# Performance work log

Hardware: AMD Instinct MI355X
Metric: run time of the kernel (lower is better)

Reference implementation:

```python
import jax, jax.numpy as jnp
import numpy as np

T, B, IN_DIM = 512, 256, 256
H1, H = 512, 256          # fc hidden, GRU hidden
OUT_DIM = 18


def setup_inputs() -> dict:
    key = jax.random.key(0)
    ks = jax.random.split(key, 14)
    s = 0.05
    return {
        "x":      jax.random.normal(ks[0], (T, B, IN_DIM), dtype=jnp.float32),
        # fc1: Linear(IN_DIM,H1)+ReLU, Linear(H1,H)+ReLU
        "W_fc1a": jax.random.normal(ks[1], (H1, IN_DIM), dtype=jnp.float32) * s,
        "b_fc1a": jax.random.normal(ks[2], (H1,), dtype=jnp.float32) * s,
        "W_fc1b": jax.random.normal(ks[3], (H, H1), dtype=jnp.float32) * s,
        "b_fc1b": jax.random.normal(ks[4], (H,), dtype=jnp.float32) * s,
        # GRUCell(H, H): weights ordered [r, z, n] like torch
        "W_ih":   jax.random.normal(ks[5], (3 * H, H), dtype=jnp.float32) * s,
        "b_ih":   jax.random.normal(ks[6], (3 * H,), dtype=jnp.float32) * s,
        "W_hh":   jax.random.normal(ks[7], (3 * H, H), dtype=jnp.float32) * s,
        "b_hh":   jax.random.normal(ks[8], (3 * H,), dtype=jnp.float32) * s,
        # fc2: Linear(H,H1)+ReLU, Linear(H1,OUT_DIM)
        "W_fc2a": jax.random.normal(ks[9], (H1, H), dtype=jnp.float32) * s,
        "b_fc2a": jax.random.normal(ks[10], (H1,), dtype=jnp.float32) * s,
        "W_fc2b": jax.random.normal(ks[11], (OUT_DIM, H1), dtype=jnp.float32) * s,
        "b_fc2b": jax.random.normal(ks[12], (OUT_DIM,), dtype=jnp.float32) * s,
    }


def reference(x, W_fc1a, b_fc1a, W_fc1b, b_fc1b,
              W_ih, b_ih, W_hh, b_hh,
              W_fc2a, b_fc2a, W_fc2b, b_fc2b):
    batch = x.shape[1]
    h0 = jnp.zeros((batch, W_hh.shape[1]), dtype=x.dtype)

    def step(h, xt):
        # fc1 MLP
        a = jax.nn.relu(xt @ W_fc1a.T + b_fc1a)
        a = jax.nn.relu(a @ W_fc1b.T + b_fc1b)
        # GRUCell (torch gate order r, z, n)
        gi = a @ W_ih.T + b_ih            # [B, 3H]
        gh = h @ W_hh.T + b_hh            # [B, 3H]
        i_r, i_z, i_n = jnp.split(gi, 3, axis=-1)
        h_r, h_z, h_n = jnp.split(gh, 3, axis=-1)
        r = jax.nn.sigmoid(i_r + h_r)
        z = jax.nn.sigmoid(i_z + h_z)
        n = jnp.tanh(i_n + r * h_n)
        h_new = (1.0 - z) * n + z * h
        # fc2 head
        q = jax.nn.relu(h_new @ W_fc2a.T + b_fc2a) @ W_fc2b.T + b_fc2b
        return h_new, q

    _, qs = jax.lax.scan(step, h0, x)     # qs: [T, B, OUT_DIM]
    return qs
```

## Files before the change

kernel.cpp:

```cpp
#include <hip/hip_runtime.h>
#include <hip/hip_fp16.h>
#include <cstdio>

typedef unsigned short u16;
typedef __attribute__((ext_vector_type(8))) _Float16 f16x8;
typedef __attribute__((ext_vector_type(4))) float fv4;

#define TT 512
#define BB 256

__device__ __forceinline__ float us2f(u16 u) {
    union { u16 u; _Float16 h; } c; c.u = u; return (float)c.h;
}
__device__ __forceinline__ u16 f2us(float f) {
    union { u16 u; _Float16 h; } c; c.h = (_Float16)f; return c.u;
}

__device__ __forceinline__ void gl_lds16(const u16* g, u16* l) {
    __builtin_amdgcn_global_load_lds(
        (const __attribute__((address_space(1))) void*)g,
        (__attribute__((address_space(3))) void*)l, 16, 0, 0);
}

__global__ void cvt_f32_f16(const float* __restrict__ s, u16* __restrict__ d, int n) {
    long stride = (long)gridDim.x * blockDim.x * 8;
    for (long i = ((long)blockIdx.x * blockDim.x + threadIdx.x) * 8; i < n; i += stride) {
        f16x8 o;
#pragma unroll
        for (int j = 0; j < 8; ++j) o[j] = (_Float16)s[i + j];
        *(f16x8*)(d + i) = o;
    }
}

__global__ void bias_fold(const float* __restrict__ bih, const float* __restrict__ bhh,
                          float* __restrict__ bsum) {
    int i = blockIdx.x * blockDim.x + threadIdx.x;
    if (i < 768) bsum[i] = bih[i] + (i < 512 ? bhh[i] : 0.f);
}

__global__ void pack_whh(const float* __restrict__ W, u16* __restrict__ Wp) {
    int t = blockIdx.x * blockDim.x + threadIdx.x;
    int l = t & 63;
    int kt = (t >> 6) & 7;
    int jt = t >> 9;
    int j = jt * 16 + (l & 15);
    int k = kt * 32 + (l >> 4) * 8;
    f16x8 o;
#pragma unroll
    for (int i = 0; i < 8; ++i) o[i] = (_Float16)W[j * 256 + k + i];
    *(f16x8*)(Wp + (size_t)t * 8) = o;
}

__global__ void pack_w2b(const float* __restrict__ W, u16* __restrict__ Wp) {
    int t = blockIdx.x * blockDim.x + threadIdx.x;
    int l = t & 63;
    int kt = (t >> 6) & 15;
    int nt = t >> 10;
    int n = nt * 16 + (l & 15);
    int k = kt * 32 + (l >> 4) * 8;
    f16x8 o;
#pragma unroll
    for (int i = 0; i < 8; ++i)
        o[i] = (n < 18) ? (_Float16)W[n * 512 + k + i] : (_Float16)0.f;
    *(f16x8*)(Wp + (size_t)t * 8) = o;
}

__global__ __launch_bounds__(256) void gemm_bt(
    const u16* __restrict__ A, const u16* __restrict__ B,
    const float* __restrict__ bias, u16* __restrict__ C,
    int N, int K, int act)
{
    __shared__ u16 Ash[4096] __attribute__((aligned(16)));
    __shared__ u16 Bsh[4096] __attribute__((aligned(16)));
    const int tid = threadIdx.x;
    const int l = tid & 63, w = tid >> 6;
    const long m0 = (long)blockIdx.y * 128;
    const int n0 = blockIdx.x * 128;
    const int r = tid >> 2, c8 = (tid & 3) * 8;
    const u16* gA0 = A + (m0 + r) * K + c8;
    const u16* gA1 = A + (m0 + 64 + r) * K + c8;
    const u16* gB0 = B + (long)(n0 + r) * K + c8;
    const u16* gB1 = B + (long)(n0 + 64 + r) * K + c8;
    const int mb = (w >> 1) * 64, nb = (w & 1) * 64;
    const int mrow = l & 15, colq = (l >> 4) * 8;
    fv4 acc[4][4] = {};
    for (int k0 = 0; k0 < K; k0 += 32) {
        gl_lds16(gA0 + k0, &Ash[tid * 8]);
        gl_lds16(gA1 + k0, &Ash[2048 + tid * 8]);
        gl_lds16(gB0 + k0, &Bsh[tid * 8]);
        gl_lds16(gB1 + k0, &Bsh[2048 + tid * 8]);
        __syncthreads();
        f16x8 af[4], bf[4];
#pragma unroll
        for (int i = 0; i < 4; ++i)
            af[i] = *(const f16x8*)&Ash[(mb + i * 16 + mrow) * 32 + colq];
#pragma unroll
        for (int i = 0; i < 4; ++i)
            bf[i] = *(const f16x8*)&Bsh[(nb + i * 16 + mrow) * 32 + colq];
#pragma unroll
        for (int mt = 0; mt < 4; ++mt)
#pragma unroll
            for (int nt = 0; nt < 4; ++nt)
                acc[mt][nt] = __builtin_amdgcn_mfma_f32_16x16x32_f16(
                    af[mt], bf[nt], acc[mt][nt], 0, 0, 0);
        __syncthreads();
    }
    float bv[4];
#pragma unroll
    for (int nt = 0; nt < 4; ++nt) bv[nt] = bias[n0 + nb + nt * 16 + mrow];
    const int rq = (l >> 4) * 4;
#pragma unroll
    for (int mt = 0; mt < 4; ++mt)
#pragma unroll
        for (int nt = 0; nt < 4; ++nt)
#pragma unroll
            for (int i = 0; i < 4; ++i) {
                float v = acc[mt][nt][i] + bv[nt];
                if (act) v = fmaxf(v, 0.f);
                C[(m0 + mb + mt * 16 + rq + i) * (long)N + (n0 + nb + nt * 16 + mrow)] = f2us(v);
            }
}

__global__ __launch_bounds__(256) void gemm_gi(
    const u16* __restrict__ A, const u16* __restrict__ B,
    const float* __restrict__ bias, u16* __restrict__ GIp)
{
    __shared__ u16 Ash[4096] __attribute__((aligned(16)));
    __shared__ u16 Bsh[4096] __attribute__((aligned(16)));
    const int tid = threadIdx.x;
    const int l = tid & 63, w = tid >> 6;
    const long m0 = (long)blockIdx.y * 128;
    const int n0 = blockIdx.x * 128;
    const int r = tid >> 2, c8 = (tid & 3) * 8;
    const u16* gA0 = A + (m0 + r) * 256 + c8;
    const u16* gA1 = A + (m0 + 64 + r) * 256 + c8;
    const u16* gB0 = B + (long)(n0 + r) * 256 + c8;
    const u16* gB1 = B + (long)(n0 + 64 + r) * 256 + c8;
    const int mb = (w >> 1) * 64, nb = (w & 1) * 64;
    const int mrow = l & 15, colq = (l >> 4) * 8;
    fv4 acc[4][4] = {};
    for (int k0 = 0; k0 < 256; k0 += 32) {
        gl_lds16(gA0 + k0, &Ash[tid * 8]);
        gl_lds16(gA1 + k0, &Ash[2048 + tid * 8]);
        gl_lds16(gB0 + k0, &Bsh[tid * 8]);
        gl_lds16(gB1 + k0, &Bsh[2048 + tid * 8]);
        __syncthreads();
        f16x8 af[4], bf[4];
#pragma unroll
        for (int i = 0; i < 4; ++i)
            af[i] = *(const f16x8*)&Ash[(mb + i * 16 + mrow) * 32 + colq];
#pragma unroll
        for (int i = 0; i < 4; ++i)
            bf[i] = *(const f16x8*)&Bsh[(nb + i * 16 + mrow) * 32 + colq];
#pragma unroll
        for (int mt = 0; mt < 4; ++mt)
#pragma unroll
            for (int nt = 0; nt < 4; ++nt)
                acc[mt][nt] = __builtin_amdgcn_mfma_f32_16x16x32_f16(
                    af[mt], bf[nt], acc[mt][nt], 0, 0, 0);
        __syncthreads();
    }
    float bv[4];
#pragma unroll
    for (int nt = 0; nt < 4; ++nt) bv[nt] = bias[n0 + nb + nt * 16 + mrow];
    const int rq = (l >> 4) * 4;
#pragma unroll
    for (int mt = 0; mt < 4; ++mt)
#pragma unroll
        for (int nt = 0; nt < 4; ++nt)
#pragma unroll
            for (int i = 0; i < 4; ++i) {
                float v = acc[mt][nt][i] + bv[nt];
                int m = (int)(m0 + mb + mt * 16 + rq + i);
                int n = n0 + nb + nt * 16 + mrow;
                int t  = m >> 8, b = m & 255;
                int blk = b >> 4, rb = b & 15, q = rb >> 2, i2 = rb & 3;
                int g = n >> 8, c = n & 255, w2 = c >> 5, s = (c >> 4) & 1, cl = c & 15;
                size_t idx = ((((size_t)t * 16 + blk) * 8 + w2) * 64 + (q * 16 + cl)) * 24
                             + (g * 2 + s) * 4 + i2;
                GIp[idx] = f2us(v);
            }
}

__global__ __launch_bounds__(512, 2) void gru_seq4(
    const u16* __restrict__ Wp, const u16* __restrict__ GIp,
    const float* __restrict__ bhh, u16* __restrict__ Hout)
{
    __shared__ u16 h_sh[2][4096] __attribute__((aligned(16)));
    __shared__ u16 Wl[24576] __attribute__((aligned(16)));
    const int tid = threadIdx.x;
    const int l = tid & 63, w = tid >> 6;
    const int blk = blockIdx.x;
    const int bg = blk * 16;
    const int col = l & 15, quad = l >> 4;

    for (int i = tid; i < 4096; i += 512) h_sh[0][i] = 0;
    for (int idx = tid; idx < 3072; idx += 512)
        *(f16x8*)&Wl[(size_t)idx * 8] =
            *(const f16x8*)&Wp[(((size_t)(idx >> 6) * 8 + 7) * 64 + (idx & 63)) * 8];

    int jts[6];
#pragma unroll
    for (int g = 0; g < 3; ++g)
#pragma unroll
        for (int s = 0; s < 2; ++s) jts[g * 2 + s] = g * 16 + 2 * w + s;

    f16x8 wf[6][7];
#pragma unroll
    for (int u = 0; u < 6; ++u)
#pragma unroll
        for (int kt = 0; kt < 7; ++kt)
            wf[u][kt] = *(const f16x8*)&Wp[(((size_t)jts[u] * 8 + kt) * 64 + l) * 8];

    float hbn[2] = { bhh[512 + 32 * w + col], bhh[512 + 32 * w + 16 + col] };

    const u16* gbase = GIp + ((size_t)(blk * 8 + w) * 64 + l) * 24;
    f16x8 gcur[3], gnxt[3];
#pragma unroll
    for (int j = 0; j < 3; ++j) gcur[j] = *(const f16x8*)(gbase + j * 8);

    float hold[2][4] = {};
    u16* hout_base = Hout + ((size_t)(bg + quad * 4) * 256) + 32 * w + col;
    __syncthreads();

    for (int t = 0; t < TT; ++t) {
        const int rd = t & 1, wr = (t + 1) & 1;
        const u16* gn = gbase + (size_t)(t < TT - 1 ? t + 1 : t) * 196608;
#pragma unroll
        for (int j = 0; j < 3; ++j) gnxt[j] = *(const f16x8*)(gn + j * 8);

        fv4 acc[6] = {};
#pragma unroll
        for (int kt = 0; kt < 7; ++kt) {
            f16x8 a = *(const f16x8*)&h_sh[rd][(kt * 64 + l) * 8];
#pragma unroll
            for (int u = 0; u < 6; ++u)
                acc[u] = __builtin_amdgcn_mfma_f32_16x16x32_f16(a, wf[u][kt], acc[u], 0, 0, 0);
        }
        {
            f16x8 a = *(const f16x8*)&h_sh[rd][(7 * 64 + l) * 8];
#pragma unroll
            for (int u = 0; u < 6; ++u) {
                f16x8 bw = *(const f16x8*)&Wl[(size_t)(jts[u] * 64 + l) * 8];
                acc[u] = __builtin_amdgcn_mfma_f32_16x16x32_f16(a, bw, acc[u], 0, 0, 0);
            }
        }
        u16* hp = hout_base + (size_t)t * 65536;
#pragma unroll
        for (int s = 0; s < 2; ++s) {
            const int q2 = s * 2 + (col >> 3);
#pragma unroll
            for (int i = 0; i < 4; ++i) {
                float pr  = (float)gcur[0][s * 4 + i] + acc[0 + s][i];
                float pz  = (float)gcur[1][s * 4 + i] + acc[2 + s][i];
                float h_n = acc[4 + s][i] + hbn[s];
                float rg = __builtin_amdgcn_rcpf(1.f + __expf(-pr));
                float zg = __builtin_amdgcn_rcpf(1.f + __expf(-pz));
                float pre = (float)gcur[2][s * 4 + i] + rg * h_n;
                float ea = __expf(-2.f * fabsf(pre));
                float th = (1.f - ea) * __builtin_amdgcn_rcpf(1.f + ea);
                float ng = (pre >= 0.f) ? th : -th;
                float hn = (1.f - zg) * ng + zg * hold[s][i];
                hold[s][i] = hn;
                u16 hu = f2us(hn);
                h_sh[wr][(w * 64 + q2 * 16 + quad * 4 + i) * 8 + (col & 7)] = hu;
                hp[(size_t)i * 256 + s * 16] = hu;
            }
        }
#pragma unroll
        for (int j = 0; j < 3; ++j) gcur[j] = gnxt[j];
        __syncthreads();
    }
}

__global__ __launch_bounds__(256) void head_gemm(
    const u16* __restrict__ Q1, const u16* __restrict__ W2p,
    const float* __restrict__ b2, float* __restrict__ out)
{
    __shared__ u16 Ash[4096] __attribute__((aligned(16)));
    __shared__ u16 Bsh[16384] __attribute__((aligned(16)));
    const int tid = threadIdx.x;
    const int l = tid & 63, w = tid >> 6;
    const long m0 = (long)blockIdx.x * 128;
    const int col = l & 15, quad = l >> 4, colq = quad * 8;
    for (int i = tid * 8; i < 16384; i += 2048)
        *(f16x8*)&Bsh[i] = *(const f16x8*)&W2p[i];
    const int r = tid >> 2, c8 = (tid & 3) * 8;
    const u16* gA0 = Q1 + (m0 + r) * 512 + c8;
    const u16* gA1 = Q1 + (m0 + 64 + r) * 512 + c8;
    fv4 acc[2][2] = {};
    for (int k0 = 0; k0 < 512; k0 += 32) {
        gl_lds16(gA0 + k0, &Ash[tid * 8]);
        gl_lds16(gA1 + k0, &Ash[2048 + tid * 8]);
        __syncthreads();
        const int kt = k0 >> 5;
        f16x8 af[2], bf[2];
#pragma unroll
        for (int mt = 0; mt < 2; ++mt)
            af[mt] = *(const f16x8*)&Ash[(w * 32 + mt * 16 + col) * 32 + colq];
#pragma unroll
        for (int nt = 0; nt < 2; ++nt)
            bf[nt] = *(const f16x8*)&Bsh[((nt * 16 + kt) * 64 + l) * 8];
#pragma unroll
        for (int mt = 0; mt < 2; ++mt)
#pragma unroll
            for (int nt = 0; nt < 2; ++nt)
                acc[mt][nt] = __builtin_amdgcn_mfma_f32_16x16x32_f16(
                    af[mt], bf[nt], acc[mt][nt], 0, 0, 0);
        __syncthreads();
    }
    const int rq = quad * 4;
#pragma unroll
    for (int nt = 0; nt < 2; ++nt) {
        int c = nt * 16 + col;
        if (c < 18) {
            float bias = b2[c];
#pragma unroll
            for (int mt = 0; mt < 2; ++mt)
#pragma unroll
                for (int i = 0; i < 4; ++i)
                    out[(m0 + w * 32 + mt * 16 + rq + i) * 18 + c] = acc[mt][nt][i] + bias;
        }
    }
}

extern "C" void kernel_launch(void* const* d_in, const int* in_sizes, int n_in,
                              void* d_out, int out_size, void* d_ws, size_t ws_size,
                              hipStream_t stream) {
    const float* x   = (const float*)d_in[0];
    const float* W1a = (const float*)d_in[1];
    const float* b1a = (const float*)d_in[2];
    const float* W1b = (const float*)d_in[3];
    const float* b1b = (const float*)d_in[4];
    const float* Wih = (const float*)d_in[5];
    const float* bih = (const float*)d_in[6];
    const float* Whh = (const float*)d_in[7];
    const float* bhh = (const float*)d_in[8];
    const float* W2a = (const float*)d_in[9];
    const float* b2a = (const float*)d_in[10];
    const float* W2b = (const float*)d_in[11];
    const float* b2b = (const float*)d_in[12];

    char* ws = (char*)d_ws;
    u16* R    = (u16*)ws;
    u16* A2b  = (u16*)(ws + 201326592);
    u16* XH   = (u16*)(ws + 268435456);
    float* bsum = (float*)(ws + 268435456 + 67108864 - 4096);
    u16* W1ah = (u16*)(ws + 335544320);
    u16* W1bh = (u16*)(ws + 335806464);
    u16* Wihh = (u16*)(ws + 336068608);
    u16* W2ah = (u16*)(ws + 336461824);
    u16* Wpk  = (u16*)(ws + 336723968);
    u16* W2p  = (u16*)(ws + 337117184);
    if (ws_size < 337149952) {
        fprintf(stderr, "kernel_launch: ws too small (%zu < 337149952)\n", ws_size);
    }

    cvt_f32_f16<<<dim3(2048), dim3(256), 0, stream>>>(x, XH, 33554432);
    cvt_f32_f16<<<dim3(64), dim3(256), 0, stream>>>(W1a, W1ah, 131072);
    cvt_f32_f16<<<dim3(64), dim3(256), 0, stream>>>(W1b, W1bh, 131072);
    cvt_f32_f16<<<dim3(96), dim3(256), 0, stream>>>(Wih, Wihh, 196608);
    cvt_f32_f16<<<dim3(64), dim3(256), 0, stream>>>(W2a, W2ah, 131072);
    pack_whh<<<dim3(96), dim3(256), 0, stream>>>(Whh, Wpk);
    pack_w2b<<<dim3(8), dim3(256), 0, stream>>>(W2b, W2p);

    gemm_bt<<<dim3(4, 1024), dim3(256), 0, stream>>>(XH, W1ah, b1a, R,   512, 256, 1);
    bias_fold<<<dim3(3), dim3(256), 0, stream>>>(bih, bhh, bsum);
    gemm_bt<<<dim3(2, 1024), dim3(256), 0, stream>>>(R,  W1bh, b1b, A2b, 256, 512, 1);
    gemm_gi<<<dim3(6, 1024), dim3(256), 0, stream>>>(A2b, Wihh, bsum, R);
    gru_seq4<<<dim3(16), dim3(512), 0, stream>>>(Wpk, R, bhh, XH);
    gemm_bt<<<dim3(4, 1024), dim3(256), 0, stream>>>(XH, W2ah, b2a, R, 512, 256, 1);
    head_gemm<<<dim3(1024), dim3(256), 0, stream>>>(R, W2p, b2b, (float*)d_out);
}
```

Measured before the change: 1.466 ms.

## Single-buffer GRU hidden state with LDS-only barriers and drop gate prefetch

The serial GRU kernel now keeps one LDS hidden-state buffer instead of double-buffering, using two barriers per step (after the MFMA reads, after the writes). These barriers wait only on the LDS/scalar counter, so outstanding global stores of H do not stall each step. The next-step prefetch of the input-gate values is replaced by an in-step load, and the occupancy hint moves to waves_per_eu. The cost is an extra barrier per step, plus global load latency for the gate values now falling on the critical path.

```diff
diff --git a/kernel.cpp b/kernel.cpp
--- a/kernel.cpp
+++ b/kernel.cpp
@@ -20,6 +20,11 @@
     __builtin_amdgcn_global_load_lds(
         (const __attribute__((address_space(1))) void*)g,
         (__attribute__((address_space(3))) void*)l, 16, 0, 0);
+}
+
+__device__ __forceinline__ void sync_lds() {
+    __builtin_amdgcn_s_waitcnt(0xC00F);
+    __builtin_amdgcn_s_barrier();
 }
 
 __global__ void cvt_f32_f16(const float* __restrict__ s, u16* __restrict__ d, int n) {
@@ -182,11 +187,12 @@
             }
 }
 
-__global__ __launch_bounds__(512, 2) void gru_seq4(
-    const u16* __restrict__ Wp, const u16* __restrict__ GIp,
-    const float* __restrict__ bhh, u16* __restrict__ Hout)
+__global__ __launch_bounds__(512)
+__attribute__((amdgpu_waves_per_eu(2, 2)))
+void gru_seq5(u16* Wp, const u16* __restrict__ GIp,
+              const float* __restrict__ bhh, u16* Hout)
 {
-    __shared__ u16 h_sh[2][4096] __attribute__((aligned(16)));
+    __shared__ u16 h_sh[4096] __attribute__((aligned(16)));
     __shared__ u16 Wl[24576] __attribute__((aligned(16)));
     const int tid = threadIdx.x;
     const int l = tid & 63, w = tid >> 6;
@@ -194,7 +200,7 @@
     const int bg = blk * 16;
     const int col = l & 15, quad = l >> 4;
 
-    for (int i = tid; i < 4096; i += 512) h_sh[0][i] = 0;
+    for (int i = tid; i < 4096; i += 512) h_sh[i] = 0;
     for (int idx = tid; idx < 3072; idx += 512)
         *(f16x8*)&Wl[(size_t)idx * 8] =
             *(const f16x8*)&Wp[(((size_t)(idx >> 6) * 8 + 7) * 64 + (idx & 63)) * 8];
@@ -215,36 +221,34 @@
     float hbn[2] = { bhh[512 + 32 * w + col], bhh[512 + 32 * w + 16 + col] };
 
     const u16* gbase = GIp + ((size_t)(blk * 8 + w) * 64 + l) * 24;
-    f16x8 gcur[3], gnxt[3];
-#pragma unroll
-    for (int j = 0; j < 3; ++j) gcur[j] = *(const f16x8*)(gbase + j * 8);
-
     float hold[2][4] = {};
     u16* hout_base = Hout + ((size_t)(bg + quad * 4) * 256) + 32 * w + col;
     __syncthreads();
 
     for (int t = 0; t < TT; ++t) {
-        const int rd = t & 1, wr = (t + 1) & 1;
-        const u16* gn = gbase + (size_t)(t < TT - 1 ? t + 1 : t) * 196608;
-#pragma unroll
-        for (int j = 0; j < 3; ++j) gnxt[j] = *(const f16x8*)(gn + j * 8);
+        const u16* gp = gbase + (size_t)t * 196608;
+        f16x8 gcur[3];
+#pragma unroll
+        for (int j = 0; j < 3; ++j) gcur[j] = *(const f16x8*)(gp + j * 8);
 
         fv4 acc[6] = {};
 #pragma unroll
         for (int kt = 0; kt < 7; ++kt) {
-            f16x8 a = *(const f16x8*)&h_sh[rd][(kt * 64 + l) * 8];
+            f16x8 a = *(const f16x8*)&h_sh[(kt * 64 + l) * 8];
 #pragma unroll
             for (int u = 0; u < 6; ++u)
                 acc[u] = __builtin_amdgcn_mfma_f32_16x16x32_f16(a, wf[u][kt], acc[u], 0, 0, 0);
         }
         {
-            f16x8 a = *(const f16x8*)&h_sh[rd][(7 * 64 + l) * 8];
+            f16x8 a = *(const f16x8*)&h_sh[(7 * 64 + l) * 8];
 #pragma unroll
             for (int u = 0; u < 6; ++u) {
                 f16x8 bw = *(const f16x8*)&Wl[(size_t)(jts[u] * 64 + l) * 8];
                 acc[u] = __builtin_amdgcn_mfma_f32_16x16x32_f16(a, bw, acc[u], 0, 0, 0);
             }
         }
+        sync_lds();
+
         u16* hp = hout_base + (size_t)t * 65536;
 #pragma unroll
         for (int s = 0; s < 2; ++s) {
@@ -263,13 +267,11 @@
                 float hn = (1.f - zg) * ng + zg * hold[s][i];
                 hold[s][i] = hn;
                 u16 hu = f2us(hn);
-                h_sh[wr][(w * 64 + q2 * 16 + quad * 4 + i) * 8 + (col & 7)] = hu;
+                h_sh[(w * 64 + q2 * 16 + quad * 4 + i) * 8 + (col & 7)] = hu;
                 hp[(size_t)i * 256 + s * 16] = hu;
             }
         }
-#pragma unroll
-        for (int j = 0; j < 3; ++j) gcur[j] = gnxt[j];
-        __syncthreads();
+        sync_lds();
     }
 }
 
@@ -368,7 +370,7 @@
     bias_fold<<<dim3(3), dim3(256), 0, stream>>>(bih, bhh, bsum);
     gemm_bt<<<dim3(2, 1024), dim3(256), 0, stream>>>(R,  W1bh, b1b, A2b, 256, 512, 1);
     gemm_gi<<<dim3(6, 1024), dim3(256), 0, stream>>>(A2b, Wihh, bsum, R);
-    gru_seq4<<<dim3(16), dim3(512), 0, stream>>>(Wpk, R, bhh, XH);
+    gru_seq5<<<dim3(16), dim3(512), 0, stream>>>(Wpk, R, bhh, XH);
     gemm_bt<<<dim3(4, 1024), dim3(256), 0, stream>>>(XH, W2ah, b2a, R, 512, 256, 1);
     head_gemm<<<dim3(1024), dim3(256), 0, stream>>>(R, W2p, b2b, (float*)d_out);
 }
```

New measurement: 1.568 ms. +6.9%, slower.
